# Kernel optimization log

Measured on AMD Instinct MI355X. Metric: run time of the kernel, lower is better.

Reference implementation:

```python
import jax, jax.numpy as jnp
import numpy as np

SIGMA = 2.0  # gaussian kernel std, matches init kwarg
N, H, W = 200, 448, 448
NUM_CLASSES = 80


def setup_inputs() -> dict:
    key = jax.random.key(0)
    k1, k2, k3 = jax.random.split(key, 3)
    seg_masks = (jax.random.uniform(k1, (N, H, W)) < 0.3).astype(jnp.float32)
    # scores in descending order (matrix_nms assumes sorted input)
    cate_scores = jnp.sort(jax.random.uniform(k2, (N,), dtype=jnp.float32))[::-1]
    cate_labels = jax.random.randint(k3, (N,), 0, NUM_CLASSES)
    return {"seg_masks": seg_masks, "cate_scores": cate_scores, "cate_labels": cate_labels}


def reference(seg_masks, cate_scores, cate_labels):
    n = seg_masks.shape[0]
    flat = seg_masks.reshape(n, -1).astype(jnp.float32)          # (n, HW)
    sum_masks = flat.sum(axis=1)                                  # (n,)
    inter = flat @ flat.T                                         # (n, n) mask intersection
    union = sum_masks[None, :] + sum_masks[:, None] - inter
    iou = jnp.triu(inter / union, k=1)                            # upper-tri IoU
    same_label = jnp.triu(
        (cate_labels[None, :] == cate_labels[:, None]).astype(jnp.float32), k=1
    )
    decay_iou = iou * same_label                                  # (n, n)
    # compensate IoU: per-candidate max overlap with a higher-scoring same-class mask
    compensate_iou = decay_iou.max(axis=0)                        # (n,)
    # gaussian decay: exp(-sigma*iou^2) / exp(-sigma*comp_i^2), min over rows
    decay_matrix = jnp.exp(SIGMA * (compensate_iou[:, None] ** 2 - decay_iou ** 2))
    decay_coefficient = decay_matrix.min(axis=0)                  # (n,)
    return cate_scores * decay_coefficient
```

## Files before the change

### kernel.cpp

```cpp
#include <hip/hip_runtime.h>
#include <cstdint>
#include <cstddef>

#define N_INST 200
#define HWPIX (448 * 448)
#define W64 3136
#define W16 12544
#define SIGMA 2.0f
#define NCHUNK 4
#define NTILE 1275

#define OFF_P   5017600
#define P_SLAB  (N_INST * N_INST)
#define OFF_SP  (OFF_P + NCHUNK * P_SLAB * 4)
#define OFF_DT  (OFF_SP + NCHUNK * 256 * 4)

__global__ void pack_kernel(const float* __restrict__ seg,
                            uint16_t* __restrict__ packed16) {
    const int mask = blockIdx.y;
    const int tid  = threadIdx.x;
    const size_t base = (size_t)mask * HWPIX + (size_t)blockIdx.x * 4096 + (size_t)tid * 16;
    const float4* s4 = (const float4*)(seg + base);
    float4 v0 = s4[0], v1 = s4[1], v2 = s4[2], v3 = s4[3];
    uint32_t m = 0;
    m |= (v0.x > 0.5f) ? 1u << 0  : 0u;  m |= (v0.y > 0.5f) ? 1u << 1  : 0u;
    m |= (v0.z > 0.5f) ? 1u << 2  : 0u;  m |= (v0.w > 0.5f) ? 1u << 3  : 0u;
    m |= (v1.x > 0.5f) ? 1u << 4  : 0u;  m |= (v1.y > 0.5f) ? 1u << 5  : 0u;
    m |= (v1.z > 0.5f) ? 1u << 6  : 0u;  m |= (v1.w > 0.5f) ? 1u << 7  : 0u;
    m |= (v2.x > 0.5f) ? 1u << 8  : 0u;  m |= (v2.y > 0.5f) ? 1u << 9  : 0u;
    m |= (v2.z > 0.5f) ? 1u << 10 : 0u;  m |= (v2.w > 0.5f) ? 1u << 11 : 0u;
    m |= (v3.x > 0.5f) ? 1u << 12 : 0u;  m |= (v3.y > 0.5f) ? 1u << 13 : 0u;
    m |= (v3.z > 0.5f) ? 1u << 14 : 0u;  m |= (v3.w > 0.5f) ? 1u << 15 : 0u;
    packed16[(size_t)mask * W16 + blockIdx.x * 256 + tid] = (uint16_t)m;
}

__global__ void pair_kernel(const uint64_t* __restrict__ packed,
                            int* __restrict__ P,
                            int* __restrict__ SP) {
    const int wt   = blockIdx.x * 4 + (threadIdx.x >> 6);
    const int lane = threadIdx.x & 63;
    const int t     = wt >> 2;
    const int chunk = wt & 3;

    int jt = (int)((sqrtf((float)(8 * t + 1)) - 1.0f) * 0.5f);
    while ((jt + 1) * (jt + 2) / 2 <= t) ++jt;
    while (jt * (jt + 1) / 2 > t) --jt;
    const int it = t - jt * (jt + 1) / 2;
    const int i0 = 4 * it, j0 = 4 * jt;

    const int ks = (chunk * 49) >> 2;
    const int ke = ((chunk + 1) * 49) >> 2;

    const uint64_t* A = packed + (size_t)i0 * W64;
    const uint64_t* B = packed + (size_t)j0 * W64;

    int c[16];
#pragma unroll
    for (int x = 0; x < 16; ++x) c[x] = 0;

    for (int kb = ks; kb < ke; ++kb) {
        const int k = kb * 64 + lane;
        uint64_t a0 = A[k], a1 = A[k + W64], a2 = A[k + 2 * W64], a3 = A[k + 3 * W64];
        uint64_t b0 = B[k], b1 = B[k + W64], b2 = B[k + 2 * W64], b3 = B[k + 3 * W64];
        c[0]  += __popcll(a0 & b0); c[1]  += __popcll(a0 & b1);
        c[2]  += __popcll(a0 & b2); c[3]  += __popcll(a0 & b3);
        c[4]  += __popcll(a1 & b0); c[5]  += __popcll(a1 & b1);
        c[6]  += __popcll(a1 & b2); c[7]  += __popcll(a1 & b3);
        c[8]  += __popcll(a2 & b0); c[9]  += __popcll(a2 & b1);
        c[10] += __popcll(a2 & b2); c[11] += __popcll(a2 & b3);
        c[12] += __popcll(a3 & b0); c[13] += __popcll(a3 & b1);
        c[14] += __popcll(a3 & b2); c[15] += __popcll(a3 & b3);
    }

    int p[8];
#pragma unroll
    for (int m = 0; m < 8; ++m) p[m] = c[2 * m] + (c[2 * m + 1] << 16);
#pragma unroll
    for (int off = 1; off < 64; off <<= 1) {
#pragma unroll
        for (int m = 0; m < 8; ++m) p[m] += __shfl_xor(p[m], off, 64);
    }

    if (lane == 0) {
#pragma unroll
        for (int r = 0; r < 4; ++r) {
#pragma unroll
            for (int cc = 0; cc < 4; ++cc) {
                const int idx = r * 4 + cc;
                const int val = (idx & 1) ? (int)(((unsigned)p[idx >> 1]) >> 16)
                                          : (p[idx >> 1] & 0xFFFF);
                const int i = i0 + r, j = j0 + cc;
                if (i < j)       P[chunk * P_SLAB + j * N_INST + i] = val;
                else if (i == j) SP[chunk * 256 + i] = val;
            }
        }
    }
}

__global__ void iou_kernel(const int* __restrict__ P,
                           const int* __restrict__ SP,
                           const int* __restrict__ labels,
                           float* __restrict__ DTf) {
    const int j = blockIdx.x;
    const int sj = SP[j] + SP[256 + j] + SP[512 + j] + SP[768 + j];
    const int lj = labels[j];
    for (int i = threadIdx.x; i < j; i += 64) {
        const int inter = P[j * N_INST + i] + P[P_SLAB + j * N_INST + i]
                        + P[2 * P_SLAB + j * N_INST + i] + P[3 * P_SLAB + j * N_INST + i];
        const int si = SP[i] + SP[256 + i] + SP[512 + i] + SP[768 + i];
        const float iou = (float)inter / (float)(si + sj - inter);
        DTf[j * N_INST + i] = (labels[i] == lj) ? iou : 0.0f;
    }
}

__global__ void finalize_kernel(const float* __restrict__ DTf,
                                const float* __restrict__ scores,
                                float* __restrict__ out) {
    __shared__ float comp[N_INST];
    const int t = threadIdx.x;
    if (t < N_INST) {
        const float* row = DTf + (size_t)t * N_INST;
        float m = 0.0f;
        for (int i = 0; i < t; ++i) m = fmaxf(m, row[i]);
        comp[t] = m;
    }
    __syncthreads();
    if (t < N_INST) {
        const float* row = DTf + (size_t)t * N_INST;
        float mn = 3.4e38f;
        for (int i = 0; i < N_INST; ++i) {
            const float ci = comp[i];
            float v = ci * ci;
            if (i < t) { const float d = row[i]; v -= d * d; }
            mn = fminf(mn, v);
        }
        out[t] = scores[t] * expf(SIGMA * mn);
    }
}

extern "C" void kernel_launch(void* const* d_in, const int* in_sizes, int n_in,
                              void* d_out, int out_size, void* d_ws, size_t ws_size,
                              hipStream_t stream) {
    const float* seg    = (const float*)d_in[0];
    const float* scores = (const float*)d_in[1];
    const int*   labels = (const int*)d_in[2];
    float* out = (float*)d_out;

    uint64_t* packed   = (uint64_t*)d_ws;
    uint16_t* packed16 = (uint16_t*)d_ws;
    int*      P        = (int*)((char*)d_ws + OFF_P);
    int*      SP       = (int*)((char*)d_ws + OFF_SP);
    float*    DTf      = (float*)((char*)d_ws + OFF_DT);

    {
        dim3 grid(49, N_INST);
        pack_kernel<<<grid, 256, 0, stream>>>(seg, packed16);
    }
    pair_kernel<<<NTILE, 256, 0, stream>>>(packed, P, SP);
    iou_kernel<<<N_INST, 64, 0, stream>>>(P, SP, labels, DTf);
    finalize_kernel<<<1, 256, 0, stream>>>(DTf, scores, out);
}
```

Baseline: 290.7 us.

## Enlarge pair tiles to 8x8 with 8 K-chunks and parallelize finalize across blocks

```diff
diff --git a/kernel.cpp b/kernel.cpp
--- a/kernel.cpp
+++ b/kernel.cpp
@@ -7,13 +7,14 @@
 #define W64 3136
 #define W16 12544
 #define SIGMA 2.0f
-#define NCHUNK 4
-#define NTILE 1275
+#define NCHUNK 8
+#define NTILE 325
 
+#define P_SLAB  (N_INST * N_INST)
 #define OFF_P   5017600
-#define P_SLAB  (N_INST * N_INST)
 #define OFF_SP  (OFF_P + NCHUNK * P_SLAB * 4)
 #define OFF_DT  (OFF_SP + NCHUNK * 256 * 4)
+#define OFF_CMP (OFF_DT + N_INST * N_INST * 4)
 
 __global__ void pack_kernel(const float* __restrict__ seg,
                             uint16_t* __restrict__ packed16) {
@@ -39,54 +40,52 @@
                             int* __restrict__ SP) {
     const int wt   = blockIdx.x * 4 + (threadIdx.x >> 6);
     const int lane = threadIdx.x & 63;
-    const int t     = wt >> 2;
-    const int chunk = wt & 3;
+    const int t     = wt >> 3;
+    const int chunk = wt & 7;
 
     int jt = (int)((sqrtf((float)(8 * t + 1)) - 1.0f) * 0.5f);
     while ((jt + 1) * (jt + 2) / 2 <= t) ++jt;
     while (jt * (jt + 1) / 2 > t) --jt;
     const int it = t - jt * (jt + 1) / 2;
-    const int i0 = 4 * it, j0 = 4 * jt;
+    const int i0 = 8 * it, j0 = 8 * jt;
 
-    const int ks = (chunk * 49) >> 2;
-    const int ke = ((chunk + 1) * 49) >> 2;
+    const int ks = (chunk * 49) >> 3;
+    const int ke = ((chunk + 1) * 49) >> 3;
 
     const uint64_t* A = packed + (size_t)i0 * W64;
     const uint64_t* B = packed + (size_t)j0 * W64;
 
-    int c[16];
+    int c[64];
 #pragma unroll
-    for (int x = 0; x < 16; ++x) c[x] = 0;
+    for (int x = 0; x < 64; ++x) c[x] = 0;
 
     for (int kb = ks; kb < ke; ++kb) {
         const int k = kb * 64 + lane;
-        uint64_t a0 = A[k], a1 = A[k + W64], a2 = A[k + 2 * W64], a3 = A[k + 3 * W64];
-        uint64_t b0 = B[k], b1 = B[k + W64], b2 = B[k + 2 * W64], b3 = B[k + 3 * W64];
-        c[0]  += __popcll(a0 & b0); c[1]  += __popcll(a0 & b1);
-        c[2]  += __popcll(a0 & b2); c[3]  += __popcll(a0 & b3);
-        c[4]  += __popcll(a1 & b0); c[5]  += __popcll(a1 & b1);
-        c[6]  += __popcll(a1 & b2); c[7]  += __popcll(a1 & b3);
-        c[8]  += __popcll(a2 & b0); c[9]  += __popcll(a2 & b1);
-        c[10] += __popcll(a2 & b2); c[11] += __popcll(a2 & b3);
-        c[12] += __popcll(a3 & b0); c[13] += __popcll(a3 & b1);
-        c[14] += __popcll(a3 & b2); c[15] += __popcll(a3 & b3);
+        uint64_t a[8], b[8];
+#pragma unroll
+        for (int r = 0; r < 8; ++r) { a[r] = A[k + r * W64]; b[r] = B[k + r * W64]; }
+#pragma unroll
+        for (int r = 0; r < 8; ++r)
+#pragma unroll
+            for (int cc = 0; cc < 8; ++cc)
+                c[r * 8 + cc] += __popcll(a[r] & b[cc]);
     }
 
-    int p[8];
+    int p[32];
 #pragma unroll
-    for (int m = 0; m < 8; ++m) p[m] = c[2 * m] + (c[2 * m + 1] << 16);
+    for (int m = 0; m < 32; ++m) p[m] = c[2 * m] + (c[2 * m + 1] << 16);
 #pragma unroll
     for (int off = 1; off < 64; off <<= 1) {
 #pragma unroll
-        for (int m = 0; m < 8; ++m) p[m] += __shfl_xor(p[m], off, 64);
+        for (int m = 0; m < 32; ++m) p[m] += __shfl_xor(p[m], off, 64);
     }
 
     if (lane == 0) {
 #pragma unroll
-        for (int r = 0; r < 4; ++r) {
+        for (int r = 0; r < 8; ++r) {
 #pragma unroll
-            for (int cc = 0; cc < 4; ++cc) {
-                const int idx = r * 4 + cc;
+            for (int cc = 0; cc < 8; ++cc) {
+                const int idx = r * 8 + cc;
                 const int val = (idx & 1) ? (int)(((unsigned)p[idx >> 1]) >> 16)
                                           : (p[idx >> 1] & 0xFFFF);
                 const int i = i0 + r, j = j0 + cc;
@@ -102,40 +101,52 @@
                            const int* __restrict__ labels,
                            float* __restrict__ DTf) {
     const int j = blockIdx.x;
-    const int sj = SP[j] + SP[256 + j] + SP[512 + j] + SP[768 + j];
+    int sj = 0;
+#pragma unroll
+    for (int cch = 0; cch < NCHUNK; ++cch) sj += SP[cch * 256 + j];
     const int lj = labels[j];
     for (int i = threadIdx.x; i < j; i += 64) {
-        const int inter = P[j * N_INST + i] + P[P_SLAB + j * N_INST + i]
-                        + P[2 * P_SLAB + j * N_INST + i] + P[3 * P_SLAB + j * N_INST + i];
-        const int si = SP[i] + SP[256 + i] + SP[512 + i] + SP[768 + i];
+        int inter = 0;
+#pragma unroll
+        for (int cch = 0; cch < NCHUNK; ++cch)
+            inter += P[cch * P_SLAB + j * N_INST + i];
+        int si = 0;
+#pragma unroll
+        for (int cch = 0; cch < NCHUNK; ++cch) si += SP[cch * 256 + i];
         const float iou = (float)inter / (float)(si + sj - inter);
         DTf[j * N_INST + i] = (labels[i] == lj) ? iou : 0.0f;
     }
 }
 
+__global__ void comp_kernel(const float* __restrict__ DTf,
+                            float* __restrict__ comp) {
+    const int j = blockIdx.x;
+    const int t = threadIdx.x;
+    const float* row = DTf + (size_t)j * N_INST;
+    float m = 0.0f;
+    for (int i = t; i < j; i += 64) m = fmaxf(m, row[i]);
+#pragma unroll
+    for (int off = 1; off < 64; off <<= 1) m = fmaxf(m, __shfl_xor(m, off, 64));
+    if (t == 0) comp[j] = m;
+}
+
 __global__ void finalize_kernel(const float* __restrict__ DTf,
+                                const float* __restrict__ comp,
                                 const float* __restrict__ scores,
                                 float* __restrict__ out) {
-    __shared__ float comp[N_INST];
+    const int j = blockIdx.x;
     const int t = threadIdx.x;
-    if (t < N_INST) {
-        const float* row = DTf + (size_t)t * N_INST;
-        float m = 0.0f;
-        for (int i = 0; i < t; ++i) m = fmaxf(m, row[i]);
-        comp[t] = m;
+    const float* row = DTf + (size_t)j * N_INST;
+    float mn = 3.4e38f;
+    for (int i = t; i < N_INST; i += 64) {
+        const float ci = comp[i];
+        float v = ci * ci;
+        if (i < j) { const float d = row[i]; v -= d * d; }
+        mn = fminf(mn, v);
     }
-    __syncthreads();
-    if (t < N_INST) {
-        const float* row = DTf + (size_t)t * N_INST;
-        float mn = 3.4e38f;
-        for (int i = 0; i < N_INST; ++i) {
-            const float ci = comp[i];
-            float v = ci * ci;
-            if (i < t) { const float d = row[i]; v -= d * d; }
-            mn = fminf(mn, v);
-        }
-        out[t] = scores[t] * expf(SIGMA * mn);
-    }
+#pragma unroll
+    for (int off = 1; off < 64; off <<= 1) mn = fminf(mn, __shfl_xor(mn, off, 64));
+    if (t == 0) out[j] = scores[j] * expf(SIGMA * mn);
 }
 
 extern "C" void kernel_launch(void* const* d_in, const int* in_sizes, int n_in,
@@ -151,12 +162,14 @@
     int*      P        = (int*)((char*)d_ws + OFF_P);
     int*      SP       = (int*)((char*)d_ws + OFF_SP);
     float*    DTf      = (float*)((char*)d_ws + OFF_DT);
+    float*    comp     = (float*)((char*)d_ws + OFF_CMP);
 
     {
         dim3 grid(49, N_INST);
         pack_kernel<<<grid, 256, 0, stream>>>(seg, packed16);
     }
-    pair_kernel<<<NTILE, 256, 0, stream>>>(packed, P, SP);
+    pair_kernel<<<(NTILE * NCHUNK + 3) / 4, 256, 0, stream>>>(packed, P, SP);
     iou_kernel<<<N_INST, 64, 0, stream>>>(P, SP, labels, DTf);
-    finalize_kernel<<<1, 256, 0, stream>>>(DTf, scores, out);
+    comp_kernel<<<N_INST, 64, 0, stream>>>(DTf, comp);
+    finalize_kernel<<<N_INST, 64, 0, stream>>>(DTf, comp, scores, out);
 }
```

Result: faster. 253.1 us (-12.9%).
